# Optimization experiments

Hardware: AMD Instinct MI355X
Metric: run time of the kernel (lower is better)

The kernel has to match this reference:

```python
import jax, jax.numpy as jnp
import numpy as np

B, H, F = 4096, 32, 1024     # batch, hp_num, feat_dim
N_CAT, CAT_DIM = 8, 16       # categorical dims 0..7, each |domain| = 16
N_CONT = H - N_CAT
LN_EPS = 1e-5


def setup_inputs() -> dict:
    key = jax.random.key(0)
    ks = jax.random.split(key, 8)
    s = 1.0 / np.sqrt(F)  # ~xavier scale
    return {
        "z": jax.random.normal(ks[0], (B, F), jnp.float32),
        "edge": jax.random.randint(ks[1], (2, 10), 0, B),
        # stacked per-hp projection Linears (weights stored as [in, out])
        "W_proj": jax.random.normal(ks[2], (H, F, F), jnp.float32) * s,
        "b_proj": jnp.zeros((H, F), jnp.float32),
        # LayerNorm over [hp_num, feat_dim]
        "ln_w": jnp.ones((H, F), jnp.float32),
        "ln_b": jnp.zeros((H, F), jnp.float32),
        # reverse_embedding for categorical dims (softmax heads)
        "W_cat": jax.random.normal(ks[3], (N_CAT, F, CAT_DIM), jnp.float32) * s,
        "b_cat": jnp.zeros((N_CAT, CAT_DIM), jnp.float32),
        # reverse_embedding for continuous dims (scalar heads)
        "W_cont": jax.random.normal(ks[4], (N_CONT, F, 1), jnp.float32) * s,
        "b_cont": jnp.zeros((N_CONT, 1), jnp.float32),
    }


def reference(z, edge, W_proj, b_proj, ln_w, ln_b, W_cat, b_cat, W_cont, b_cont):
    # per-hp projection: batched GEMM replacing batch*hp_num tiny Linears
    latent = jnp.einsum('bf,hfd->bhd', z, W_proj) + b_proj  # [B, H, F]
    # LayerNorm normalized over the last two dims [hp_num, feat_dim]
    mu = latent.mean(axis=(1, 2), keepdims=True)
    var = latent.var(axis=(1, 2), keepdims=True)
    latent = (latent - mu) * jax.lax.rsqrt(var + LN_EPS) * ln_w + ln_b
    latent = jax.nn.relu(latent)
    # reverse embeddings: categorical heads (dims 0..N_CAT-1) get softmax
    cat_logits = jnp.einsum('bhf,hfc->bhc', latent[:, :N_CAT], W_cat) + b_cat
    pred_cat = jax.nn.softmax(cat_logits, axis=-1)          # [B, N_CAT, CAT_DIM]
    pred_cont = jnp.einsum('bhf,hfc->bhc', latent[:, N_CAT:], W_cont) + b_cont  # [B, N_CONT, 1]
    return pred_cat, pred_cont, latent
```

## Files before the change

### kernel.cpp

```cpp
#include <hip/hip_runtime.h>

typedef unsigned short u16;
typedef __bf16 bf16x8 __attribute__((ext_vector_type(8)));
typedef float f32x4 __attribute__((ext_vector_type(4)));

#define B_SZ   4096
#define H_NUM  32
#define F_DIM  1024
#define NTOT   (H_NUM * F_DIM)
#define N_CAT  8
#define CAT_D  16
#define N_CONT 24
#define LN_EPS 1e-5f
#define NSTRIP 128

__device__ __forceinline__ u16 f2bf(float f) {
    unsigned int u = __builtin_bit_cast(unsigned int, f);
    unsigned int r = (u + 0x7FFFu + ((u >> 16) & 1u)) >> 16;
    return (u16)r;
}

__device__ __forceinline__ float bf2f(u16 v) {
    unsigned int u = ((unsigned int)v) << 16;
    return __builtin_bit_cast(float, u);
}

__device__ __forceinline__ void gl2lds16(const void* g, void* l) {
    __builtin_amdgcn_global_load_lds(
        (const __attribute__((address_space(1))) void*)g,
        (__attribute__((address_space(3))) void*)l,
        16, 0, 0);
}

__device__ __forceinline__ float wave_sum(float v) {
#pragma unroll
    for (int o = 32; o; o >>= 1) v += __shfl_xor(v, o);
    return v;
}

__global__ __launch_bounds__(256) void zconv(const float* __restrict__ z,
                                             u16* __restrict__ zb) {
    int i = blockIdx.x * 256 + threadIdx.x;
    float4 v = ((const float4*)z)[i];
    ushort4 o;
    o.x = f2bf(v.x); o.y = f2bf(v.y); o.z = f2bf(v.z); o.w = f2bf(v.w);
    ((ushort4*)zb)[i] = o;
}

__global__ __launch_bounds__(256) void transpose_w(const float* __restrict__ W,
                                                   u16* __restrict__ Wt) {
    __shared__ u16 tile[64][72];
    const int h = blockIdx.z;
    const int f0 = blockIdx.x * 64;
    const int d0 = blockIdx.y * 64;
    const float* Wh = W + (size_t)h * F_DIM * F_DIM;
    u16* Wth = Wt + (size_t)h * F_DIM * F_DIM;
    const int t = threadIdx.x;

#pragma unroll
    for (int i = 0; i < 4; ++i) {
        int idx = i * 256 + t;
        int fr = idx >> 4;
        int c4 = idx & 15;
        float4 v = *(const float4*)(Wh + (size_t)(f0 + fr) * F_DIM + d0 + c4 * 4);
        tile[fr][c4 * 4 + 0] = f2bf(v.x);
        tile[fr][c4 * 4 + 1] = f2bf(v.y);
        tile[fr][c4 * 4 + 2] = f2bf(v.z);
        tile[fr][c4 * 4 + 3] = f2bf(v.w);
    }
    __syncthreads();
#pragma unroll
    for (int i = 0; i < 2; ++i) {
        int idx = i * 256 + t;
        int dr = idx >> 3;
        int c8 = idx & 7;
        __attribute__((aligned(16))) u16 tmp[8];
#pragma unroll
        for (int j = 0; j < 8; ++j) tmp[j] = tile[c8 * 8 + j][dr];
        *(uint4*)(Wth + (size_t)(d0 + dr) * F_DIM + f0 + c8 * 8) = *(const uint4*)tmp;
    }
}

template <int BF>
__global__ __launch_bounds__(512, 2) void gemm256(const u16* __restrict__ A,
                                                  const u16* __restrict__ Bt,
                                                  const float* __restrict__ bproj,
                                                  u16* __restrict__ lat16,
                                                  float* __restrict__ latf,
                                                  float* __restrict__ psum,
                                                  float* __restrict__ psumsq) {
    extern __shared__ u16 dynlds[];
    const int t = threadIdx.x;
    const int wid = t >> 6;
    const int lane = t & 63;
    const int l16 = lane & 15;
    const int lk = lane >> 4;
    const int wm = wid >> 2;
    const int wn = wid & 3;

    const int wg = blockIdx.x;
    const int xcd = wg & 7;
    const int local = wg >> 3;
    const int m0 = (local & 15) * 256;
    const int n0 = ((xcd << 4) + (local >> 4)) * 256;

    f32x4 acc[8][4];
    const f32x4 zero = {0.f, 0.f, 0.f, 0.f};
#pragma unroll
    for (int m = 0; m < 8; ++m)
#pragma unroll
        for (int n = 0; n < 4; ++n) acc[m][n] = zero;

    auto stage = [&](int p, int ktn, int bn) {
        const char* srcbase = (p < 2) ? (const char*)A : (const char*)Bt;
        const int rowbase = (p < 2) ? (m0 + p * 128) : (n0 + (p - 2) * 128);
        u16* ldsbase = dynlds + bn * 32768 + (p >> 1) * 16384 + (p & 1) * 8192;
#pragma unroll
        for (int i = 0; i < 2; ++i) {
            int oo = i * 8192 + t * 16;
            int oos = oo ^ (((oo >> 7) & 7) << 4);
            int row = oo >> 7;
            int colb = oos & 127;
            gl2lds16(srcbase + (size_t)(rowbase + row) * 2048 + ktn * 128 + colb,
                     ldsbase + i * 4096 + (wid << 9));
        }
    };

#pragma unroll
    for (int p = 0; p < 4; ++p) stage(p, 0, 0);
    __syncthreads();

    const int swz = (l16 & 7) << 4;
    for (int kt = 0; kt < 16; ++kt) {
        const int buf = kt & 1;
        const char* aB = (const char*)(dynlds + buf * 32768 + wm * 8192);
        const char* bB = (const char*)(dynlds + buf * 32768 + 16384 + (wn >> 1) * 8192);
        bf16x8 bfr[4][2];
#pragma unroll
        for (int p = 0; p < 4; ++p) {
            if (kt < 15) stage(p, kt + 1, buf ^ 1);
            if (p == 0) {
#pragma unroll
                for (int nr = 0; nr < 4; ++nr)
#pragma unroll
                    for (int kk = 0; kk < 2; ++kk)
                        bfr[nr][kk] = *(const bf16x8*)(bB +
                            ((wn & 1) * 64 + nr * 16 + l16) * 128 +
                            ((kk * 64 + lk * 16) ^ swz));
            }
            bf16x8 afr[2][2];
#pragma unroll
            for (int mr = 0; mr < 2; ++mr)
#pragma unroll
                for (int kk = 0; kk < 2; ++kk)
                    afr[mr][kk] = *(const bf16x8*)(aB +
                        (p * 32 + mr * 16 + l16) * 128 +
                        ((kk * 64 + lk * 16) ^ swz));
            __builtin_amdgcn_s_setprio(1);
#pragma unroll
            for (int kk = 0; kk < 2; ++kk)
#pragma unroll
                for (int mr = 0; mr < 2; ++mr)
#pragma unroll
                    for (int nr = 0; nr < 4; ++nr)
                        acc[p * 2 + mr][nr] = __builtin_amdgcn_mfma_f32_16x16x32_bf16(
                            afr[mr][kk], bfr[nr][kk], acc[p * 2 + mr][nr], 0, 0, 0);
            __builtin_amdgcn_s_setprio(0);
        }
        __syncthreads();
    }

    float bias[4];
#pragma unroll
    for (int nr = 0; nr < 4; ++nr) bias[nr] = bproj[n0 + wn * 64 + nr * 16 + l16];

    float sm[8][4], s2[8][4];
#pragma unroll
    for (int mr = 0; mr < 8; ++mr)
#pragma unroll
        for (int j = 0; j < 4; ++j) { sm[mr][j] = 0.f; s2[mr][j] = 0.f; }

#pragma unroll
    for (int mr = 0; mr < 8; ++mr) {
#pragma unroll
        for (int j = 0; j < 4; ++j) {
            const int rowg = m0 + wm * 128 + mr * 16 + lk * 4 + j;
            size_t off = (size_t)rowg * NTOT + n0 + wn * 64 + l16;
#pragma unroll
            for (int nr = 0; nr < 4; ++nr) {
                float v = acc[mr][nr][j] + bias[nr];
                if (BF) lat16[off + nr * 16] = f2bf(v);
                else    latf[off + nr * 16] = v;
                sm[mr][j] += v;
                s2[mr][j] += v * v;
            }
        }
    }
#pragma unroll
    for (int o = 1; o < 16; o <<= 1) {
#pragma unroll
        for (int mr = 0; mr < 8; ++mr)
#pragma unroll
            for (int j = 0; j < 4; ++j) {
                sm[mr][j] += __shfl_xor(sm[mr][j], o);
                s2[mr][j] += __shfl_xor(s2[mr][j], o);
            }
    }
    float* sredf = (float*)dynlds;
    float* s2f   = sredf + 1024;
    __syncthreads();
    if (l16 == 0) {
#pragma unroll
        for (int mr = 0; mr < 8; ++mr)
#pragma unroll
            for (int j = 0; j < 4; ++j) {
                int r = wm * 128 + mr * 16 + lk * 4 + j;
                sredf[wn * 256 + r] = sm[mr][j];
                s2f[wn * 256 + r] = s2[mr][j];
            }
    }
    __syncthreads();
    if (t < 256) {
        const int strip = n0 >> 8;
        float S = sredf[t] + sredf[256 + t] + sredf[512 + t] + sredf[768 + t];
        float S2 = s2f[t] + s2f[256 + t] + s2f[512 + t] + s2f[768 + t];
        psum[(size_t)strip * B_SZ + m0 + t] = S;
        psumsq[(size_t)strip * B_SZ + m0 + t] = S2;
    }
}

__global__ __launch_bounds__(256) void ln_finalize(const float* __restrict__ psum,
                                                   const float* __restrict__ psumsq,
                                                   float* __restrict__ murs) {
    const int t = threadIdx.x;
    const int b0 = blockIdx.x * 64;
    const int tb = t & 63;
    const int tg = t >> 6;
    float s = 0.f, s2 = 0.f;
    for (int sidx = tg; sidx < NSTRIP; sidx += 4) {
        s += psum[(size_t)sidx * B_SZ + b0 + tb];
        s2 += psumsq[(size_t)sidx * B_SZ + b0 + tb];
    }
    __shared__ float r1[4][64], r2[4][64];
    r1[tg][tb] = s;
    r2[tg][tb] = s2;
    __syncthreads();
    if (t < 64) {
        float S = r1[0][t] + r1[1][t] + r1[2][t] + r1[3][t];
        float S2 = r2[0][t] + r2[1][t] + r2[2][t] + r2[3][t];
        float m = S / (float)NTOT;
        float var = S2 / (float)NTOT - m * m;
        murs[b0 + t] = m;
        murs[B_SZ + b0 + t] = rsqrtf(var + LN_EPS);
    }
}

template <int BF>
__global__ __launch_bounds__(256) void headsI(const void* __restrict__ latin_,
                                              float* __restrict__ latout,
                                              const float* __restrict__ murs,
                                              const float* __restrict__ lnw,
                                              const float* __restrict__ lnb,
                                              const float* __restrict__ Wcat,
                                              const float* __restrict__ bcat,
                                              const float* __restrict__ Wcont,
                                              const float* __restrict__ bcont,
                                              float* __restrict__ pcat,
                                              float* __restrict__ pcont) {
    const int half = blockIdx.x;
    const int b = blockIdx.y;
    const int t = threadIdx.x;
    const int lane = t & 63;
    const int w4 = t >> 6;
    const float mu = murs[b];
    const float rs = murs[B_SZ + b];
    const ushort4* lin16 = (const ushort4*)((const u16*)latin_ + (size_t)b * NTOT);
    const float4*  linf  = (const float4*)((const float*)latin_ + (size_t)b * NTOT);
    f32x4* lout4 = (f32x4*)(latout + (size_t)b * NTOT);
    const float4* lnw4 = (const float4*)lnw;
    const float4* lnb4 = (const float4*)lnb;
    const float4* wcont4 = (const float4*)Wcont;

    __shared__ ushort4 sy16[N_CAT * 256];
    __shared__ float4 cred4[4][N_CAT][4];
    __shared__ float nred[16][4];

    const int kbase = half << 4;
    float cp[16];

#pragma unroll 4
    for (int kk = 0; kk < 16; ++kk) {
        const int k = kbase + kk;
        const int i = (k << 8) + t;
        float4 x;
        if (BF) {
            ushort4 xv = lin16[i];
            x.x = bf2f(xv.x); x.y = bf2f(xv.y); x.z = bf2f(xv.z); x.w = bf2f(xv.w);
        } else {
            x = linf[i];
        }
        float4 w = lnw4[i];
        float4 bv = lnb4[i];
        float4 yo;
        yo.x = fmaxf(0.f, (x.x - mu) * rs * w.x + bv.x);
        yo.y = fmaxf(0.f, (x.y - mu) * rs * w.y + bv.y);
        yo.z = fmaxf(0.f, (x.z - mu) * rs * w.z + bv.z);
        yo.w = fmaxf(0.f, (x.w - mu) * rs * w.w + bv.w);
        f32x4 yv = {yo.x, yo.y, yo.z, yo.w};
        __builtin_nontemporal_store(yv, lout4 + i);
        if (half == 0 && k < N_CAT) {
            ushort4 ys;
            ys.x = f2bf(yo.x); ys.y = f2bf(yo.y); ys.z = f2bf(yo.z); ys.w = f2bf(yo.w);
            sy16[i] = ys;
            cp[kk] = 0.f;
        } else {
            float4 wv = wcont4[((k - N_CAT) << 8) + t];
            cp[kk] = yo.x * wv.x + yo.y * wv.y + yo.z * wv.z + yo.w * wv.w;
        }
    }
    __syncthreads();

    if (half == 0) {
        const int cq = t & 3;
        const int fg = t >> 2;
        for (int k = 0; k < N_CAT; ++k) {
            const float4* Wc4 = (const float4*)(Wcat + (size_t)k * F_DIM * CAT_D);
            float4 a4 = {0.f, 0.f, 0.f, 0.f};
#pragma unroll
            for (int jq = 0; jq < 4; ++jq) {
                ushort4 yv = sy16[(k << 8) + fg * 4 + jq];
                float ys[4] = {bf2f(yv.x), bf2f(yv.y), bf2f(yv.z), bf2f(yv.w)};
#pragma unroll
                for (int r = 0; r < 4; ++r) {
                    int f = fg * 16 + jq * 4 + r;
                    float4 wv = Wc4[f * 4 + cq];
                    a4.x += ys[r] * wv.x;
                    a4.y += ys[r] * wv.y;
                    a4.z += ys[r] * wv.z;
                    a4.w += ys[r] * wv.w;
                }
            }
#pragma unroll
            for (int o = 4; o < 64; o <<= 1) {
                a4.x += __shfl_xor(a4.x, o);
                a4.y += __shfl_xor(a4.y, o);
                a4.z += __shfl_xor(a4.z, o);
                a4.w += __shfl_xor(a4.w, o);
            }
            if (lane < 4) cred4[w4][k][lane] = a4;
        }
#pragma unroll
        for (int kk = 8; kk < 16; ++kk) {
            float v = wave_sum(cp[kk]);
            if (lane == 0) nred[kk - 8][w4] = v;
        }
    } else {
#pragma unroll
        for (int kk = 0; kk < 16; ++kk) {
            float v = wave_sum(cp[kk]);
            if (lane == 0) nred[kk][w4] = v;
        }
    }
    __syncthreads();

    if (half == 0) {
        if (t < 128) {
            const int h = t >> 4, c = t & 15;
            float lg = bcat[h * CAT_D + c];
#pragma unroll
            for (int w = 0; w < 4; ++w)
                lg += ((const float*)cred4[w][h])[c];
            float mx = lg;
#pragma unroll
            for (int o = 8; o; o >>= 1) mx = fmaxf(mx, __shfl_xor(mx, o, 16));
            float e = __expf(lg - mx);
            float sm2 = e;
#pragma unroll
            for (int o = 8; o; o >>= 1) sm2 += __shfl_xor(sm2, o, 16);
            pcat[(size_t)b * (N_CAT * CAT_D) + t] = e / sm2;
        } else if (t >= 128 && t < 128 + 8) {
            const int ci = t - 128;
            pcont[(size_t)b * N_CONT + ci] =
                nred[ci][0] + nred[ci][1] + nred[ci][2] + nred[ci][3] + bcont[ci];
        }
    } else {
        if (t < 16) {
            const int ci = 8 + t;
            pcont[(size_t)b * N_CONT + ci] =
                nred[t][0] + nred[t][1] + nred[t][2] + nred[t][3] + bcont[ci];
        }
    }
}

extern "C" void kernel_launch(void* const* d_in, const int* in_sizes, int n_in,
                              void* d_out, int out_size, void* d_ws, size_t ws_size,
                              hipStream_t stream) {
    const float* z     = (const float*)d_in[0];
    const float* Wp    = (const float*)d_in[2];
    const float* bp    = (const float*)d_in[3];
    const float* lnw   = (const float*)d_in[4];
    const float* lnb   = (const float*)d_in[5];
    const float* Wcat  = (const float*)d_in[6];
    const float* bcat  = (const float*)d_in[7];
    const float* Wcont = (const float*)d_in[8];
    const float* bcont = (const float*)d_in[9];

    float* out    = (float*)d_out;
    float* pcat   = out;
    float* pcont  = out + (size_t)B_SZ * N_CAT * CAT_D;
    float* latent = pcont + (size_t)B_SZ * N_CONT;

    u16* zb     = (u16*)d_ws;
    u16* Wt     = zb + (size_t)B_SZ * F_DIM;
    float* murs = (float*)(Wt + (size_t)NTOT * F_DIM);
    float* psum   = murs + 2 * B_SZ;
    float* psumsq = psum + (size_t)B_SZ * NSTRIP;
    u16* lat16  = (u16*)(psumsq + (size_t)B_SZ * NSTRIP);

    const size_t need = (size_t)((char*)(lat16 + (size_t)B_SZ * NTOT) - (char*)d_ws);
    const bool usebf = ws_size >= need;

    const int LDSB = 131072;
    zconv<<<dim3(B_SZ * F_DIM / 1024), 256, 0, stream>>>(z, zb);
    transpose_w<<<dim3(16, 16, 32), 256, 0, stream>>>(Wp, Wt);
    if (usebf) {
        (void)hipFuncSetAttribute((const void*)gemm256<1>,
                                  hipFuncAttributeMaxDynamicSharedMemorySize, LDSB);
        gemm256<1><<<dim3(2048), 512, LDSB, stream>>>(zb, Wt, bp, lat16, nullptr,
                                                      psum, psumsq);
        ln_finalize<<<dim3(B_SZ / 64), 256, 0, stream>>>(psum, psumsq, murs);
        headsI<1><<<dim3(2, B_SZ), 256, 0, stream>>>(lat16, latent, murs, lnw, lnb,
                                                     Wcat, bcat, Wcont, bcont, pcat, pcont);
    } else {
        (void)hipFuncSetAttribute((const void*)gemm256<0>,
                                  hipFuncAttributeMaxDynamicSharedMemorySize, LDSB);
        gemm256<0><<<dim3(2048), 512, LDSB, stream>>>(zb, Wt, bp, nullptr, latent,
                                                      psum, psumsq);
        ln_finalize<<<dim3(B_SZ / 64), 256, 0, stream>>>(psum, psumsq, murs);
        headsI<0><<<dim3(2, B_SZ), 256, 0, stream>>>(latent, latent, murs, lnw, lnb,
                                                     Wcat, bcat, Wcont, bcont, pcat, pcont);
    }
}
```

Measured before the change: 777.7 us.

## Pack LayerNorm params and Wcont to bf16, merge heads kernel halves per row

Adds a pre-pass that packs ln_w/ln_b into interleaved bf16 pairs and converts W_cont to bf16, so the heads kernel reads half the parameter bytes per row. The heads kernel now uses one block per batch row covering all 32 hp slices instead of two half-blocks, and latent is written with plain stores instead of nontemporal ones. The costs are an extra small launch, bf16 rounding of the LN affine parameters and W_cont (a precision change), fewer and longer blocks, and more registers for 24 partial sums.

Measured after the change: 704.5 us. 1.1x faster.

```diff
diff --git a/kernel.cpp b/kernel.cpp
--- a/kernel.cpp
+++ b/kernel.cpp
@@ -1,6 +1,7 @@
 #include <hip/hip_runtime.h>
 
 typedef unsigned short u16;
+typedef unsigned int u32;
 typedef __bf16 bf16x8 __attribute__((ext_vector_type(8)));
 typedef float f32x4 __attribute__((ext_vector_type(4)));
 
@@ -25,6 +26,9 @@
     return __builtin_bit_cast(float, u);
 }
 
+__device__ __forceinline__ float bflo(u32 v) { return bf2f((u16)(v & 0xffffu)); }
+__device__ __forceinline__ float bfhi(u32 v) { return bf2f((u16)(v >> 16)); }
+
 __device__ __forceinline__ void gl2lds16(const void* g, void* l) {
     __builtin_amdgcn_global_load_lds(
         (const __attribute__((address_space(1))) void*)g,
@@ -45,6 +49,30 @@
     ushort4 o;
     o.x = f2bf(v.x); o.y = f2bf(v.y); o.z = f2bf(v.z); o.w = f2bf(v.w);
     ((ushort4*)zb)[i] = o;
+}
+
+__global__ __launch_bounds__(256) void packln(const float* __restrict__ lnw,
+                                              const float* __restrict__ lnb,
+                                              const float* __restrict__ wcont,
+                                              uint4* __restrict__ lnwb,
+                                              ushort4* __restrict__ wc16) {
+    int idx = blockIdx.x * 256 + threadIdx.x;
+    if (idx < NTOT / 4) {
+        float4 w = ((const float4*)lnw)[idx];
+        float4 b = ((const float4*)lnb)[idx];
+        uint4 o;
+        o.x = (u32)f2bf(w.x) | ((u32)f2bf(w.y) << 16);
+        o.y = (u32)f2bf(w.z) | ((u32)f2bf(w.w) << 16);
+        o.z = (u32)f2bf(b.x) | ((u32)f2bf(b.y) << 16);
+        o.w = (u32)f2bf(b.z) | ((u32)f2bf(b.w) << 16);
+        lnwb[idx] = o;
+    } else if (idx < NTOT / 4 + N_CONT * F_DIM / 4) {
+        int j = idx - NTOT / 4;
+        float4 v = ((const float4*)wcont)[j];
+        ushort4 o;
+        o.x = f2bf(v.x); o.y = f2bf(v.y); o.z = f2bf(v.z); o.w = f2bf(v.w);
+        wc16[j] = o;
+    }
 }
 
 __global__ __launch_bounds__(256) void transpose_w(const float* __restrict__ W,
@@ -256,19 +284,17 @@
 }
 
 template <int BF>
-__global__ __launch_bounds__(256) void headsI(const void* __restrict__ latin_,
+__global__ __launch_bounds__(256) void headsJ(const void* __restrict__ latin_,
                                               float* __restrict__ latout,
                                               const float* __restrict__ murs,
-                                              const float* __restrict__ lnw,
-                                              const float* __restrict__ lnb,
+                                              const uint4* __restrict__ lnwb,
+                                              const ushort4* __restrict__ wc16,
                                               const float* __restrict__ Wcat,
                                               const float* __restrict__ bcat,
-                                              const float* __restrict__ Wcont,
                                               const float* __restrict__ bcont,
                                               float* __restrict__ pcat,
                                               float* __restrict__ pcont) {
-    const int half = blockIdx.x;
-    const int b = blockIdx.y;
+    const int b = blockIdx.x;
     const int t = threadIdx.x;
     const int lane = t & 63;
     const int w4 = t >> 6;
@@ -276,21 +302,16 @@
     const float rs = murs[B_SZ + b];
     const ushort4* lin16 = (const ushort4*)((const u16*)latin_ + (size_t)b * NTOT);
     const float4*  linf  = (const float4*)((const float*)latin_ + (size_t)b * NTOT);
-    f32x4* lout4 = (f32x4*)(latout + (size_t)b * NTOT);
-    const float4* lnw4 = (const float4*)lnw;
-    const float4* lnb4 = (const float4*)lnb;
-    const float4* wcont4 = (const float4*)Wcont;
+    float4* lout4 = (float4*)(latout + (size_t)b * NTOT);
 
     __shared__ ushort4 sy16[N_CAT * 256];
     __shared__ float4 cred4[4][N_CAT][4];
-    __shared__ float nred[16][4];
-
-    const int kbase = half << 4;
-    float cp[16];
-
-#pragma unroll 4
-    for (int kk = 0; kk < 16; ++kk) {
-        const int k = kbase + kk;
+    __shared__ float nred[N_CONT][4];
+
+    float cp[N_CONT];
+
+#pragma unroll 2
+    for (int k = 0; k < N_CAT; ++k) {
         const int i = (k << 8) + t;
         float4 x;
         if (BF) {
@@ -299,96 +320,94 @@
         } else {
             x = linf[i];
         }
-        float4 w = lnw4[i];
-        float4 bv = lnb4[i];
+        uint4 wb = lnwb[i];
         float4 yo;
-        yo.x = fmaxf(0.f, (x.x - mu) * rs * w.x + bv.x);
-        yo.y = fmaxf(0.f, (x.y - mu) * rs * w.y + bv.y);
-        yo.z = fmaxf(0.f, (x.z - mu) * rs * w.z + bv.z);
-        yo.w = fmaxf(0.f, (x.w - mu) * rs * w.w + bv.w);
-        f32x4 yv = {yo.x, yo.y, yo.z, yo.w};
-        __builtin_nontemporal_store(yv, lout4 + i);
-        if (half == 0 && k < N_CAT) {
-            ushort4 ys;
-            ys.x = f2bf(yo.x); ys.y = f2bf(yo.y); ys.z = f2bf(yo.z); ys.w = f2bf(yo.w);
-            sy16[i] = ys;
-            cp[kk] = 0.f;
+        yo.x = fmaxf(0.f, (x.x - mu) * rs * bflo(wb.x) + bflo(wb.z));
+        yo.y = fmaxf(0.f, (x.y - mu) * rs * bfhi(wb.x) + bfhi(wb.z));
+        yo.z = fmaxf(0.f, (x.z - mu) * rs * bflo(wb.y) + bflo(wb.w));
+        yo.w = fmaxf(0.f, (x.w - mu) * rs * bfhi(wb.y) + bfhi(wb.w));
+        lout4[i] = yo;
+        ushort4 ys;
+        ys.x = f2bf(yo.x); ys.y = f2bf(yo.y); ys.z = f2bf(yo.z); ys.w = f2bf(yo.w);
+        sy16[i] = ys;
+    }
+
+#pragma unroll 2
+    for (int k = N_CAT; k < H_NUM; ++k) {
+        const int i = (k << 8) + t;
+        float4 x;
+        if (BF) {
+            ushort4 xv = lin16[i];
+            x.x = bf2f(xv.x); x.y = bf2f(xv.y); x.z = bf2f(xv.z); x.w = bf2f(xv.w);
         } else {
-            float4 wv = wcont4[((k - N_CAT) << 8) + t];
-            cp[kk] = yo.x * wv.x + yo.y * wv.y + yo.z * wv.z + yo.w * wv.w;
-        }
-    }
-    __syncthreads();
-
-    if (half == 0) {
-        const int cq = t & 3;
-        const int fg = t >> 2;
-        for (int k = 0; k < N_CAT; ++k) {
-            const float4* Wc4 = (const float4*)(Wcat + (size_t)k * F_DIM * CAT_D);
-            float4 a4 = {0.f, 0.f, 0.f, 0.f};
-#pragma unroll
-            for (int jq = 0; jq < 4; ++jq) {
-                ushort4 yv = sy16[(k << 8) + fg * 4 + jq];
-                float ys[4] = {bf2f(yv.x), bf2f(yv.y), bf2f(yv.z), bf2f(yv.w)};
-#pragma unroll
-                for (int r = 0; r < 4; ++r) {
-                    int f = fg * 16 + jq * 4 + r;
-                    float4 wv = Wc4[f * 4 + cq];
-                    a4.x += ys[r] * wv.x;
-                    a4.y += ys[r] * wv.y;
-                    a4.z += ys[r] * wv.z;
-                    a4.w += ys[r] * wv.w;
-                }
+            x = linf[i];
+        }
+        uint4 wb = lnwb[i];
+        ushort4 wv = wc16[((k - N_CAT) << 8) + t];
+        float4 yo;
+        yo.x = fmaxf(0.f, (x.x - mu) * rs * bflo(wb.x) + bflo(wb.z));
+        yo.y = fmaxf(0.f, (x.y - mu) * rs * bfhi(wb.x) + bfhi(wb.z));
+        yo.z = fmaxf(0.f, (x.z - mu) * rs * bflo(wb.y) + bflo(wb.w));
+        yo.w = fmaxf(0.f, (x.w - mu) * rs * bfhi(wb.y) + bfhi(wb.w));
+        lout4[i] = yo;
+        cp[k - N_CAT] = yo.x * bf2f(wv.x) + yo.y * bf2f(wv.y) +
+                        yo.z * bf2f(wv.z) + yo.w * bf2f(wv.w);
+    }
+    __syncthreads();
+
+    const int cq = t & 3;
+    const int fg = t >> 2;
+    for (int k = 0; k < N_CAT; ++k) {
+        const float4* Wc4 = (const float4*)(Wcat + (size_t)k * F_DIM * CAT_D);
+        float4 a4 = {0.f, 0.f, 0.f, 0.f};
+#pragma unroll
+        for (int jq = 0; jq < 4; ++jq) {
+            ushort4 yv = sy16[(k << 8) + fg * 4 + jq];
+            float ys[4] = {bf2f(yv.x), bf2f(yv.y), bf2f(yv.z), bf2f(yv.w)};
+#pragma unroll
+            for (int r = 0; r < 4; ++r) {
+                int f = fg * 16 + jq * 4 + r;
+                float4 wv = Wc4[f * 4 + cq];
+                a4.x += ys[r] * wv.x;
+                a4.y += ys[r] * wv.y;
+                a4.z += ys[r] * wv.z;
+                a4.w += ys[r] * wv.w;
             }
-#pragma unroll
-            for (int o = 4; o < 64; o <<= 1) {
-                a4.x += __shfl_xor(a4.x, o);
-                a4.y += __shfl_xor(a4.y, o);
-                a4.z += __shfl_xor(a4.z, o);
-                a4.w += __shfl_xor(a4.w, o);
-            }
-            if (lane < 4) cred4[w4][k][lane] = a4;
-        }
-#pragma unroll
-        for (int kk = 8; kk < 16; ++kk) {
-            float v = wave_sum(cp[kk]);
-            if (lane == 0) nred[kk - 8][w4] = v;
-        }
-    } else {
-#pragma unroll
-        for (int kk = 0; kk < 16; ++kk) {
-            float v = wave_sum(cp[kk]);
-            if (lane == 0) nred[kk][w4] = v;
-        }
-    }
-    __syncthreads();
-
-    if (half == 0) {
-        if (t < 128) {
-            const int h = t >> 4, c = t & 15;
-            float lg = bcat[h * CAT_D + c];
-#pragma unroll
-            for (int w = 0; w < 4; ++w)
-                lg += ((const float*)cred4[w][h])[c];
-            float mx = lg;
-#pragma unroll
-            for (int o = 8; o; o >>= 1) mx = fmaxf(mx, __shfl_xor(mx, o, 16));
-            float e = __expf(lg - mx);
-            float sm2 = e;
-#pragma unroll
-            for (int o = 8; o; o >>= 1) sm2 += __shfl_xor(sm2, o, 16);
-            pcat[(size_t)b * (N_CAT * CAT_D) + t] = e / sm2;
-        } else if (t >= 128 && t < 128 + 8) {
-            const int ci = t - 128;
-            pcont[(size_t)b * N_CONT + ci] =
-                nred[ci][0] + nred[ci][1] + nred[ci][2] + nred[ci][3] + bcont[ci];
-        }
-    } else {
-        if (t < 16) {
-            const int ci = 8 + t;
-            pcont[(size_t)b * N_CONT + ci] =
-                nred[t][0] + nred[t][1] + nred[t][2] + nred[t][3] + bcont[ci];
-        }
+        }
+#pragma unroll
+        for (int o = 4; o < 64; o <<= 1) {
+            a4.x += __shfl_xor(a4.x, o);
+            a4.y += __shfl_xor(a4.y, o);
+            a4.z += __shfl_xor(a4.z, o);
+            a4.w += __shfl_xor(a4.w, o);
+        }
+        if (lane < 4) cred4[w4][k][lane] = a4;
+    }
+#pragma unroll
+    for (int k = 0; k < N_CONT; ++k) {
+        float v = wave_sum(cp[k]);
+        if (lane == 0) nred[k][w4] = v;
+    }
+    __syncthreads();
+
+    if (t < 128) {
+        const int h = t >> 4, c = t & 15;
+        float lg = bcat[h * CAT_D + c];
+#pragma unroll
+        for (int w = 0; w < 4; ++w)
+            lg += ((const float*)cred4[w][h])[c];
+        float mx = lg;
+#pragma unroll
+        for (int o = 8; o; o >>= 1) mx = fmaxf(mx, __shfl_xor(mx, o, 16));
+        float e = __expf(lg - mx);
+        float sm2 = e;
+#pragma unroll
+        for (int o = 8; o; o >>= 1) sm2 += __shfl_xor(sm2, o, 16);
+        pcat[(size_t)b * (N_CAT * CAT_D) + t] = e / sm2;
+    } else if (t >= 128 && t < 128 + N_CONT) {
+        const int ci = t - 128;
+        pcont[(size_t)b * N_CONT + ci] =
+            nred[ci][0] + nred[ci][1] + nred[ci][2] + nred[ci][3] + bcont[ci];
     }
 }
 
@@ -415,13 +434,17 @@
     float* murs = (float*)(Wt + (size_t)NTOT * F_DIM);
     float* psum   = murs + 2 * B_SZ;
     float* psumsq = psum + (size_t)B_SZ * NSTRIP;
-    u16* lat16  = (u16*)(psumsq + (size_t)B_SZ * NSTRIP);
+    uint4* lnwb = (uint4*)(psumsq + (size_t)B_SZ * NSTRIP);
+    ushort4* wc16 = (ushort4*)(lnwb + NTOT / 4);
+    u16* lat16  = (u16*)(wc16 + N_CONT * F_DIM / 4);
 
     const size_t need = (size_t)((char*)(lat16 + (size_t)B_SZ * NTOT) - (char*)d_ws);
     const bool usebf = ws_size >= need;
 
     const int LDSB = 131072;
     zconv<<<dim3(B_SZ * F_DIM / 1024), 256, 0, stream>>>(z, zb);
+    packln<<<dim3((NTOT / 4 + N_CONT * F_DIM / 4 + 255) / 256), 256, 0, stream>>>(
+        lnw, lnb, Wcont, lnwb, wc16);
     transpose_w<<<dim3(16, 16, 32), 256, 0, stream>>>(Wp, Wt);
     if (usebf) {
         (void)hipFuncSetAttribute((const void*)gemm256<1>,
@@ -429,15 +452,15 @@
         gemm256<1><<<dim3(2048), 512, LDSB, stream>>>(zb, Wt, bp, lat16, nullptr,
                                                       psum, psumsq);
         ln_finalize<<<dim3(B_SZ / 64), 256, 0, stream>>>(psum, psumsq, murs);
-        headsI<1><<<dim3(2, B_SZ), 256, 0, stream>>>(lat16, latent, murs, lnw, lnb,
-                                                     Wcat, bcat, Wcont, bcont, pcat, pcont);
+        headsJ<1><<<dim3(B_SZ), 256, 0, stream>>>(lat16, latent, murs, lnwb, wc16,
+                                                  Wcat, bcat, bcont, pcat, pcont);
     } else {
         (void)hipFuncSetAttribute((const void*)gemm256<0>,
                                   hipFuncAttributeMaxDynamicSharedMemorySize, LDSB);
         gemm256<0><<<dim3(2048), 512, LDSB, stream>>>(zb, Wt, bp, nullptr, latent,
                                                       psum, psumsq);
         ln_finalize<<<dim3(B_SZ / 64), 256, 0, stream>>>(psum, psumsq, murs);
-        headsI<0><<<dim3(2, B_SZ), 256, 0, stream>>>(latent, latent, murs, lnw, lnb,
-                                                     Wcat, bcat, Wcont, bcont, pcat, pcont);
-    }
-}
+        headsJ<0><<<dim3(B_SZ), 256, 0, stream>>>(latent, latent, murs, lnwb, wc16,
+                                                  Wcat, bcat, bcont, pcat, pcont);
+    }
+}
```
